# Kernel optimization log

Hardware: AMD Instinct MI355X
Metric: run time of the kernel (lower is better)

## Reference

```python
import jax, jax.numpy as jnp
import numpy as np

N, D, H, K, P = 1536, 1024, 16, 64, 8
FREQ_DIM = 14 * 3 * 128  # freq_embedding(pos, 128) flattened


def freq_embedding(t, size):
    # min_freq=0.01, max_freq=2**8 as in the block's call sites
    nf = size // 2
    freqs = (2.0 ** jnp.linspace(np.log2(0.01), np.log2(256.0), nf)).astype(jnp.float32)
    r = t[..., None] * freqs
    return jnp.stack((jnp.sin(r), jnp.cos(r)), axis=-1).reshape(t.shape[0], -1)


def layer_norm(x, eps=1e-5):
    m = jnp.mean(x, -1, keepdims=True)
    v = jnp.var(x, -1, keepdims=True)
    return (x - m) * jax.lax.rsqrt(v + eps)


def cond_norm(x, cond, ws, bs, wb, bb):
    return jax.nn.sigmoid(cond @ ws + bs) * layer_norm(x) + (cond @ wb + bb)


def _unit(v):
    return v * jax.lax.rsqrt(jnp.sum(v * v, -1, keepdims=True) + 1e-8)


def aa_frames(pos):
    # Gram-Schmidt frame from backbone N/CA/C (atom14 slots 0,1,2)
    n, ca, c = pos[:, 0], pos[:, 1], pos[:, 2]
    e1 = _unit(c - ca)
    v2 = n - ca
    e2 = _unit(v2 - jnp.sum(e1 * v2, -1, keepdims=True) * e1)
    e3 = jnp.cross(e1, e2)
    R = jnp.stack([e1, e2, e3], axis=-1)  # [N,3,3]
    return R, ca


def setup_inputs():
    key = jax.random.key(0)
    ks = iter(jax.random.split(key, 64))
    r = lambda *s: jax.random.normal(next(ks), s, jnp.float32)
    w = lambda *s: 0.02 * jax.random.normal(next(ks), s, jnp.float32)
    z = lambda *s: jnp.zeros(s, jnp.float32)
    return dict(
        local=r(N, D), pos=r(N, 14, 3), condition=r(N, D),
        mask=jnp.ones((N,), bool), pair_bias=r(H, N, N),
        w_f1=w(FREQ_DIM, 2 * D), b_f1=z(2 * D), w_f2=w(2 * D, D), b_f2=z(D),
        cn1_ws=w(D, D), cn1_bs=z(D), cn1_wb=w(D, D), cn1_bb=z(D),
        wq=w(D, H * K), wk=w(D, H * K), wv=w(D, H * K),
        wqp=w(D, H * P * 3), wkp=w(D, H * P * 3), wvp=w(D, H * P * 3),
        gamma=z(H), wo=w(H * (K + 4 * P), D), bo=z(D),
        cn2_ws=w(D, D), cn2_bs=z(D), cn2_wb=w(D, D), cn2_bb=z(D),
        wg1=w(D, 2 * D), bg1=z(2 * D), wg2=w(D, 2 * D), bg2=z(2 * D),
        wg3=w(2 * D, D), bg3=z(D),
        cn3_ws=w(D, D), cn3_bs=z(D), cn3_wb=w(D, D), cn3_bb=z(D),
        w_vel=w(D, 14 * 3),
    )


def reference(local, pos, condition, mask, pair_bias,
              w_f1, b_f1, w_f2, b_f2,
              cn1_ws, cn1_bs, cn1_wb, cn1_bb,
              wq, wk, wv, wqp, wkp, wvp, gamma, wo, bo,
              cn2_ws, cn2_bs, cn2_wb, cn2_bb,
              wg1, bg1, wg2, bg2, wg3, bg3,
              cn3_ws, cn3_bs, cn3_wb, cn3_bb, w_vel):
    n = local.shape[0]
    # embed_pred_pos: MLP over freq embedding of coords
    emb = freq_embedding(pos, 128)  # [N, 5376]
    local = local + (jax.nn.silu(emb @ w_f1 + b_f1) @ w_f2 + b_f2)
    # attention branch
    ai = cond_norm(local, condition, cn1_ws, cn1_bs, cn1_wb, cn1_bb)
    R, t = aa_frames(pos)
    q = (ai @ wq).reshape(n, H, K)
    k = (ai @ wk).reshape(n, H, K)
    v = (ai @ wv).reshape(n, H, K)
    to_glob = lambda p: jnp.einsum('nab,nhpb->nhpa', R, p) + t[:, None, None, :]
    qg = to_glob((ai @ wqp).reshape(n, H, P, 3))
    kg = to_glob((ai @ wkp).reshape(n, H, P, 3))
    vg = to_glob((ai @ wvp).reshape(n, H, P, 3))
    qk = jnp.einsum('ihk,jhk->hij', q, k) / np.sqrt(K).astype(np.float32)
    # squared point distances via norm expansion (never materialize [H,N,N,P,3])
    ptdot = jnp.einsum('ihpc,jhpc->hij', qg, kg)
    qn = jnp.sum(qg * qg, axis=(-1, -2)).T  # [H,N]
    kn = jnp.sum(kg * kg, axis=(-1, -2)).T
    dist2 = qn[:, :, None] + kn[None if False else slice(None), None, :] - 2.0 * ptdot
    wc = np.sqrt(2.0 / (9.0 * P)).astype(np.float32)
    logits = qk + pair_bias - 0.5 * wc * jax.nn.softplus(gamma)[:, None, None] * dist2
    logits = jnp.where(mask[None, None, :], logits, -1e9)
    a = jax.nn.softmax(logits, axis=-1)  # [H,N,N]
    o = jnp.einsum('hij,jhk->ihk', a, v).reshape(n, H * K)
    opg = jnp.einsum('hij,jhpc->ihpc', a, vg)
    opl = jnp.einsum('nba,nhpb->nhpa', R, opg - t[:, None, None, :])
    onorm = jnp.sqrt(jnp.sum(opl * opl, -1) + 1e-8).reshape(n, -1)
    upd = jnp.concatenate([o, opl.reshape(n, -1), onorm], axis=-1) @ wo + bo
    local = local + upd
    # gated MLP branch
    x = cond_norm(local, condition, cn2_ws, cn2_bs, cn2_wb, cn2_bb)
    local = local + (jax.nn.silu(x @ wg1 + bg1) * (x @ wg2 + bg2)) @ wg3 + bg3
    # output heads
    ln = cond_norm(local, condition, cn3_ws, cn3_bs, cn3_wb, cn3_bb)
    velocity = (ln @ w_vel).reshape(n, 14, 3)
    return local, velocity
```

## Files before the change

### kernel.cpp

```cpp
#include <hip/hip_runtime.h>
#include <hip/hip_bf16.h>
#include <math.h>

#define NRES 1536
#define NH 16
#define NNF 2359296ull
#define LOG2E 1.44269504f
#define KVS 4

typedef unsigned short u16;
typedef __attribute__((ext_vector_type(8))) short short8;
typedef __attribute__((ext_vector_type(4))) unsigned short u16x4;
typedef __attribute__((ext_vector_type(4))) float f32x4;

typedef const __attribute__((address_space(1))) void gvoid;
typedef __attribute__((address_space(3))) void lvoid;

__device__ __forceinline__ u16 f2b(float x){
    __hip_bfloat16 h = __float2bfloat16(x);
    return *reinterpret_cast<u16*>(&h);
}
__device__ __forceinline__ float b2f(u16 u){
    unsigned v = ((unsigned)u) << 16;
    return __uint_as_float(v);
}

#define F_BIAS  1
#define F_SILU  2
#define F_RESID 8
#define F_OUTBF 16

template<int TNF>
__global__ __launch_bounds__(256) void gemm_t(
    const u16* __restrict__ A, int lda, size_t zsA,
    const u16* __restrict__ BT, int ldb, size_t zsB,
    float* __restrict__ Cf, u16* __restrict__ Cb, int ldc, size_t zsC,
    const float* __restrict__ bias, size_t zsBias,
    const float* __restrict__ resid, int ldr, size_t zsR,
    int Ncols, int Kd, int flags, int ksl)
{
    constexpr int TN = TNF * 32;
    __shared__ u16 As[2][128 * 64];
    __shared__ u16 Bs[2][TN * 64];

    unsigned gx = gridDim.x, gy = gridDim.y;
    unsigned nb = gx * gy * gridDim.z;
    unsigned bid = (blockIdx.z * gy + blockIdx.y) * gx + blockIdx.x;
    if ((nb & 7u) == 0u) bid = (bid & 7u) * (nb >> 3) + (bid >> 3);
    const int bxi = bid % gx;
    const int byi = (bid / gx) % gy;
    const int bz  = bid / (gx * gy);

    const int tid = threadIdx.x;
    const int l = tid & 63, w = tid >> 6;
    const int bm = byi * 128, bn = bxi * TN;

    A  += zsA * bz;
    BT += zsB * bz;

    const int kbeg = ksl ? bz * ksl : 0;
    const int kend = ksl ? kbeg + ksl : Kd;
    const int nk = (kend - kbeg) >> 6;

    const int arow   = l >> 3;
    const int aslot  = l & 7;
    const int srcslt = aslot ^ arow;

    const u16* aBase[4];
    const u16* bBase[TN / 32];
    #pragma unroll
    for (int t = 0; t < 4; ++t) {
        int ra = bm + (w * 4 + t) * 8 + arow;
        aBase[t] = A + (size_t)ra * lda + srcslt * 8;
    }
    #pragma unroll
    for (int t = 0; t < TN / 32; ++t) {
        int rb = bn + (w * (TN / 32) + t) * 8 + arow;
        if (rb > Ncols - 1) rb = Ncols - 1;
        bBase[t] = BT + (size_t)rb * ldb + srcslt * 8;
    }

    const int wr = w >> 1, wc = w & 1;
    const int fr = l & 15;
    const int fq = l >> 4;

    f32x4 acc[4][TNF];
    #pragma unroll
    for (int i = 0; i < 4; ++i)
        #pragma unroll
        for (int j = 0; j < TNF; ++j) acc[i][j] = (f32x4){0.f, 0.f, 0.f, 0.f};

// ... 264 lines not shown

        float alpha[4];
        #pragma unroll
        for (int r = 0; r < 4; ++r) {
            float v = fmaxf(fmaxf(sacc[0][r], sacc[1][r]), fmaxf(sacc[2][r], sacc[3][r]));
            v = fmaxf(v, __shfl_xor(v, 1, 64));
            v = fmaxf(v, __shfl_xor(v, 2, 64));
            v = fmaxf(v, __shfl_xor(v, 4, 64));
            v = fmaxf(v, __shfl_xor(v, 8, 64));
            float mn = fmaxf(m_run[r], v);
            alpha[r] = exp2f((m_run[r] - mn) * LOG2E);
            m_run[r] = mn;
        }

        float psum[4] = {0.f, 0.f, 0.f, 0.f};
        #pragma unroll
        for (int n = 0; n < 4; ++n) {
            int col = n * 16 + fr;
            #pragma unroll
            for (int r = 0; r < 4; ++r) {
                float p = exp2f((sacc[n][r] - m_run[r]) * LOG2E);
                psum[r] += p;
                int rowf = w * 16 + fq * 4 + r;
                int byte = rowf * 128 + (((col >> 3) ^ (rowf & 7)) * 16) + (col & 7) * 2;
                *(u16*)((char*)Ps + byte) = f2b(p);
            }
        }
        #pragma unroll
        for (int r = 0; r < 4; ++r) {
            float v = psum[r];
            v += __shfl_xor(v, 1, 64);
            v += __shfl_xor(v, 2, 64);
            v += __shfl_xor(v, 4, 64);
            v += __shfl_xor(v, 8, 64);
            l_run[r] = l_run[r] * alpha[r] + v;
        }
        #pragma unroll
        for (int n = 0; n < 6; ++n)
            #pragma unroll
            for (int r = 0; r < 4; ++r)
                oacc[n][r] *= alpha[r];

        #pragma unroll
        for (int kk = 0; kk < 2; ++kk) {
            int prow = w * 16 + fr;
            short8 pa = *(const short8*)((const char*)Ps + prow * 128
                                         + (((kk * 4 + fq) ^ (prow & 7)) * 16));
            #pragma unroll
            for (int n = 0; n < 6; ++n) {
                int vrow = n * 16 + fr;
                short8 vv = *(const short8*)((const char*)Vs[cur] + vrow * 128
                                             + (((kk * 4 + fq) ^ (fr & 7)) * 16));
                oacc[n] = __builtin_amdgcn_mfma_f32_16x16x32_bf16(pa, vv, oacc[n], 0, 0, 0);
            }
        }

        __syncthreads();
        cur ^= 1;
        #pragma unroll
        for (int n = 0; n < 4; ++n) pbv[n] = pbn[n];
    }

    u16* Oz = Opart + ((size_t)z * NH + h) * NRES * 96;
    #pragma unroll
    for (int n = 0; n < 6; ++n) {
        int c = n * 16 + fr;
        #pragma unroll
        for (int r = 0; r < 4; ++r) {
            int row = q0 + w * 16 + fq * 4 + r;
            Oz[(size_t)row * 96 + c] = f2b(oacc[n][r]);
        }
    }
    if (fr == 0) {
        float* mlz = mlpart + ((size_t)z * NH + h) * NRES * 2;
        #pragma unroll
        for (int r = 0; r < 4; ++r) {
            int row = q0 + w * 16 + fq * 4 + r;
            mlz[row * 2 + 0] = m_run[r];
            mlz[row * 2 + 1] = l_run[r];
        }
    }
}

__global__ __launch_bounds__(256) void combine_kernel(
    const u16* __restrict__ Opart, const float* __restrict__ mlpart,
    float* __restrict__ cat)
{
    int idx = blockIdx.x * 256 + threadIdx.x;
    if (idx >= NH * NRES * 88) return;
    int c = idx % 88;
    int rh = idx / 88;
    float m[KVS], lv[KVS];
    float mm = -1e30f;
    #pragma unroll
    for (int s = 0; s < KVS; ++s) {
        size_t rr = (size_t)s * NH * NRES + rh;
        m[s] = mlpart[rr * 2];
        lv[s] = mlpart[rr * 2 + 1];
        mm = fmaxf(mm, m[s]);
    }
    float ll = 0.f, ov = 0.f;
    #pragma unroll
    for (int s = 0; s < KVS; ++s) {
        float wgt = exp2f((m[s] - mm) * LOG2E);
        ll += lv[s] * wgt;
        ov += b2f(Opart[((size_t)s * NH * NRES + rh) * 96 + c]) * wgt;
    }
    cat[(size_t)rh * 88 + c] = ov / ll;
}

struct TP9 { const float* p[9]; };

__global__ __launch_bounds__(256) void transpose_bz(
    TP9 tp, int ldi, size_t zsi,
    u16* __restrict__ out, int ldo, size_t zso, int K, int N, int nsrc)
{
    __shared__ float t[32][33];
    int z = blockIdx.z;
    const float* in = tp.p[(z < nsrc) ? z : 0] + zsi * ((z < nsrc) ? 0 : z);
    if (nsrc == 1) in = tp.p[0] + zsi * z;
    out += zso * z;
    int k0 = blockIdx.y * 32, n0 = blockIdx.x * 32;
    int tx = threadIdx.x & 31, ty = threadIdx.x >> 5;
    #pragma unroll
    for (int j = 0; j < 4; ++j) {
        int k = k0 + ty + j * 8;
        if (k < K && n0 + tx < N) t[ty + j * 8][tx] = in[(size_t)k * ldi + n0 + tx];
    }
    __syncthreads();
    #pragma unroll
    for (int j = 0; j < 4; ++j) {
        int n = n0 + ty + j * 8;
        int k = k0 + tx;
        if (n < N && k < K) out[(size_t)n * ldo + k] = f2b(t[tx][ty + j * 8]);
    }
}

__global__ __launch_bounds__(256) void f2b8_kernel(const float* __restrict__ in, u16* __restrict__ out, int n8)
{
    int i = blockIdx.x * 256 + threadIdx.x;
    if (i >= n8) return;
    size_t i0 = (size_t)i * 8;
    const float4* p = (const float4*)(in + i0);
    float4 a = p[0], b = p[1];
    short8 o;
    o[0]=(short)f2b(a.x); o[1]=(short)f2b(a.y); o[2]=(short)f2b(a.z); o[3]=(short)f2b(a.w);
    o[4]=(short)f2b(b.x); o[5]=(short)f2b(b.y); o[6]=(short)f2b(b.z); o[7]=(short)f2b(b.w);
    *(short8*)(out + i0) = o;
}

__global__ __launch_bounds__(256) void emb_kernel(const float* __restrict__ pos, u16* __restrict__ emb)
{
    int idx = blockIdx.x * 256 + threadIdx.x;
    int f = idx & 63;
    int rest = idx >> 6;
    int coord = rest % 42;
    int n = rest / 42;
    float t = pos[(size_t)n * 42 + coord];
    const double l0 = -6.643856189774724;
    const double step = 14.643856189774724 / 63.0;
    float freq = exp2f((float)(l0 + f * step));
    float r = t * freq;
    size_t o = (size_t)n * 5376 + (size_t)coord * 128 + 2 * f;
    emb[o]     = f2b(sinf(r));
    emb[o + 1] = f2b(cosf(r));
}

__global__ __launch_bounds__(256) void frames_kernel(const float* __restrict__ pos,
                                                     float* __restrict__ Rb, float* __restrict__ tb)
{
    int n = blockIdx.x * 256 + threadIdx.x;
    if (n >= NRES) return;
    const float* p = pos + (size_t)n * 42;
    float nx = p[0], ny = p[1], nz = p[2];
    float cax = p[3], cay = p[4], caz = p[5];
    float cx = p[6], cy = p[7], cz = p[8];
    float v1x = cx - cax, v1y = cy - cay, v1z = cz - caz;
    float i1 = rsqrtf(v1x * v1x + v1y * v1y + v1z * v1z + 1e-8f);
    float e1x = v1x * i1, e1y = v1y * i1, e1z = v1z * i1;
    float v2x = nx - cax, v2y = ny - cay, v2z = nz - caz;
    float d = e1x * v2x + e1y * v2y + e1z * v2z;
    float wx = v2x - d * e1x, wy = v2y - d * e1y, wz = v2z - d * e1z;
    float i2 = rsqrtf(wx * wx + wy * wy + wz * wz + 1e-8f);
    float e2x = wx * i2, e2y = wy * i2, e2z = wz * i2;
    float e3x = e1y * e2z - e1z * e2y;
    float e3y = e1z * e2x - e1x * e2z;
    float e3z = e1x * e2y - e1y * e2x;
    float* R = Rb + (size_t)n * 9;
    R[0] = e1x; R[1] = e2x; R[2] = e3x;
    R[3] = e1y; R[4] = e2y; R[5] = e3y;
    R[6] = e1z; R[7] = e2z; R[8] = e3z;
    tb[(size_t)n * 3 + 0] = cax;
    tb[(size_t)n * 3 + 1] = cay;
    tb[(size_t)n * 3 + 2] = caz;
}

__global__ __launch_bounds__(256) void bias_pack(const float* a, const float* b, const float* c,
                                                 const float* d, const float* e, const float* f,
                                                 float* out)
{
    int i = blockIdx.x * 256 + threadIdx.x;
    if (i >= 1024) return;
    out[i] = a[i]; out[1024 + i] = b[i]; out[2048 + i] = c[i];
    out[3072 + i] = d[i]; out[4096 + i] = e[i]; out[5120 + i] = f[i];
}

__global__ __launch_bounds__(256) void biasg_pack(const float* a, const float* b, float* out)
{
    int i = blockIdx.x * 256 + threadIdx.x;
    if (i >= 2048) return;
    out[i] = a[i]; out[2048 + i] = b[i];
}

__global__ __launch_bounds__(256) void glu_kernel(const u16* __restrict__ g12, u16* __restrict__ gm)
{
    int i = blockIdx.x * 256 + threadIdx.x;
    if (i >= NRES * 2048 / 8) return;
    size_t i0 = (size_t)i * 8;
    short8 a8 = *(const short8*)(g12 + i0);
    short8 b8 = *(const short8*)(g12 + (size_t)NRES * 2048 + i0);
    short8 o;
    #pragma unroll
    for (int j = 0; j < 8; ++j) {
        float a = b2f((u16)a8[j]);
        float b = b2f((u16)b8[j]);
        float s = a / (1.f + expf(-a));
        o[j] = (short)f2b(s * b);
    }
    *(short8*)(gm + i0) = o;
}

__global__ __launch_bounds__(256) void pack_qk(const float* __restrict__ qb, const float* __restrict__ kb,
                                               u16* __restrict__ qe, u16* __restrict__ ke)
{
    int idx = blockIdx.x * 256 + threadIdx.x;
    if (idx >= NH * NRES * 16) return;
    int g = idx & 15;
    int t = idx >> 4;
    int n = t % NRES;
    int h = t / NRES;
    size_t o = ((size_t)h * NRES + n) * 128 + g * 8;
    if (g < 8) {
        const float4* q4 = (const float4*)(qb + (size_t)n * 1024 + h * 64 + g * 8);
        const float4* k4 = (const float4*)(kb + (size_t)n * 1024 + h * 64 + g * 8);
        float4 qa = q4[0], qb2 = q4[1], ka = k4[0], kb2 = k4[1];
        short8 oq, ok;
        oq[0]=(short)f2b(0.125f*qa.x); oq[1]=(short)f2b(0.125f*qa.y);
        oq[2]=(short)f2b(0.125f*qa.z); oq[3]=(short)f2b(0.125f*qa.w);
        oq[4]=(short)f2b(0.125f*qb2.x); oq[5]=(short)f2b(0.125f*qb2.y);
        oq[6]=(short)f2b(0.125f*qb2.z); oq[7]=(short)f2b(0.125f*qb2.w);
        ok[0]=(short)f2b(ka.x); ok[1]=(short)f2b(ka.y); ok[2]=(short)f2b(ka.z); ok[3]=(short)f2b(ka.w);
        ok[4]=(short)f2b(kb2.x); ok[5]=(short)f2b(kb2.y); ok[6]=(short)f2b(kb2.z); ok[7]=(short)f2b(kb2.w);
        *(short8*)(qe + o) = oq;
        *(short8*)(ke + o) = ok;
    } else if (g >= 11) {
        short8 zz = {};
        *(short8*)(qe + o) = zz;
        *(short8*)(ke + o) = zz;
    }
}

__global__ __launch_bounds__(256) void build_pts(
    const float* __restrict__ qp, const float* __restrict__ kp, const float* __restrict__ vp,
    const float* __restrict__ Rb, const float* __restrict__ tb, const float* __restrict__ gamma,
    u16* __restrict__ qe, u16* __restrict__ ke, float* __restrict__ vgt)
{
    int idx = blockIdx.x * 256 + threadIdx.x;
    if (idx >= NRES * NH) return;
    int n = idx >> 4, h = idx & 15;
    float R[9];
    #pragma unroll
    for (int a = 0; a < 9; ++a) R[a] = Rb[(size_t)n * 9 + a];
    float t0 = tb[(size_t)n * 3 + 0], t1 = tb[(size_t)n * 3 + 1], t2 = tb[(size_t)n * 3 + 2];
    float g = gamma[h];
    float sp = (g > 20.f) ? g : log1pf(expf(g));
    float ch = 0.5f * (1.f / 6.f) * sp;

    u16* qeh = qe + ((size_t)h * NRES + n) * 128;
    u16* keh = ke + ((size_t)h * NRES + n) * 128;
    size_t pbase = (size_t)n * 384 + h * 24;
    float kn = 0.f;
    #pragma unroll
    for (int p = 0; p < 8; ++p) {
        size_t o = pbase + p * 3;
        {
            float x = qp[o], y = qp[o + 1], z = qp[o + 2];
            float g0 = R[0] * x + R[1] * y + R[2] * z + t0;
            float g1 = R[3] * x + R[4] * y + R[5] * z + t1;
            float g2 = R[6] * x + R[7] * y + R[8] * z + t2;
            qeh[64 + p * 3 + 0] = f2b(2.f * ch * g0);
            qeh[64 + p * 3 + 1] = f2b(2.f * ch * g1);
            qeh[64 + p * 3 + 2] = f2b(2.f * ch * g2);
        }
        {
            float x = kp[o], y = kp[o + 1], z = kp[o + 2];
            float g0 = R[0] * x + R[1] * y + R[2] * z + t0;
            float g1 = R[3] * x + R[4] * y + R[5] * z + t1;
            float g2 = R[6] * x + R[7] * y + R[8] * z + t2;
            keh[64 + p * 3 + 0] = f2b(g0);
            keh[64 + p * 3 + 1] = f2b(g1);
            keh[64 + p * 3 + 2] = f2b(g2);
            kn += g0 * g0 + g1 * g1 + g2 * g2;
        }
        {
            float x = vp[o], y = vp[o + 1], z = vp[o + 2];
            vgt[o]     = R[0] * x + R[1] * y + R[2] * z + t0;
            vgt[o + 1] = R[3] * x + R[4] * y + R[5] * z + t1;
            vgt[o + 2] = R[6] * x + R[7] * y + R[8] * z + t2;
        }
    }
    qeh[88] = f2b(1.0f);
    keh[88] = f2b(-ch * kn);
}

__global__ __launch_bounds__(256) void finalize_kernel(const float* __restrict__ cat,
                                                       const float* __restrict__ Rb,
                                                       const float* __restrict__ tb,
                                                       u16* __restrict__ featB)
{
    int idx = blockIdx.x * 256 + threadIdx.x;
    if (idx >= NRES * NH) return;
    int n = idx >> 4, h = idx & 15;
    float R[9];
    #pragma unroll
    for (int a = 0; a < 9; ++a) R[a] = Rb[(size_t)n * 9 + a];
    float t0 = tb[(size_t)n * 3 + 0], t1 = tb[(size_t)n * 3 + 1], t2 = tb[(size_t)n * 3 + 2];
    const float* c = cat + ((size_t)h * NRES + n) * 88;
    u16* fb = featB + (size_t)n * 1536;
    #pragma unroll
    for (int k = 0; k < 64; ++k) fb[h * 64 + k] = f2b(c[k]);
    #pragma unroll
    for (int p = 0; p < 8; ++p) {
        float x = c[64 + p * 3 + 0] - t0;
        float y = c[64 + p * 3 + 1] - t1;
        float z = c[64 + p * 3 + 2] - t2;
        float a0 = R[0] * x + R[3] * y + R[6] * z;
        float a1 = R[1] * x + R[4] * y + R[7] * z;
        float a2 = R[2] * x + R[5] * y + R[8] * z;
        fb[1024 + h * 24 + p * 3 + 0] = f2b(a0);
        fb[1024 + h * 24 + p * 3 + 1] = f2b(a1);
        fb[1024 + h * 24 + p * 3 + 2] = f2b(a2);
        fb[1408 + h * 8 + p] = f2b(sqrtf(a0 * a0 + a1 * a1 + a2 * a2 + 1e-8f));
    }
}

extern "C" void kernel_launch(void* const* d_in, const int* in_sizes, int n_in,
                              void* d_out, int out_size, void* d_ws, size_t ws_size,
                              hipStream_t stream)
{
    const float* local_in = (const float*)d_in[0];
    const float* pos      = (const float*)d_in[1];
    const float* cond     = (const float*)d_in[2];
    const float* pb       = (const float*)d_in[4];
    const float* w_f1     = (const float*)d_in[5];
    const float* b_f1     = (const float*)d_in[6];
    const float* w_f2     = (const float*)d_in[7];
    const float* b_f2     = (const float*)d_in[8];
    const float* cn1_ws   = (const float*)d_in[9];
    const float* cn1_bs   = (const float*)d_in[10];
    const float* cn1_wb   = (const float*)d_in[11];
    const float* cn1_bb   = (const float*)d_in[12];
    const float* wq       = (const float*)d_in[13];
    const float* wk       = (const float*)d_in[14];
    const float* wv       = (const float*)d_in[15];
    const float* wqp      = (const float*)d_in[16];
    const float* wkp      = (const float*)d_in[17];
    const float* wvp      = (const float*)d_in[18];
    const float* gamma    = (const float*)d_in[19];
    const float* wo       = (const float*)d_in[20];
    const float* bo       = (const float*)d_in[21];
    const float* cn2_ws   = (const float*)d_in[22];
    const float* cn2_bs   = (const float*)d_in[23];
    const float* cn2_wb   = (const float*)d_in[24];
    const float* cn2_bb   = (const float*)d_in[25];
    const float* wg1      = (const float*)d_in[26];
    const float* bg1      = (const float*)d_in[27];
    const float* wg2      = (const float*)d_in[28];
    const float* bg2      = (const float*)d_in[29];
    const float* wg3      = (const float*)d_in[30];
    const float* bg3      = (const float*)d_in[31];
    const float* cn3_ws   = (const float*)d_in[32];
    const float* cn3_bs   = (const float*)d_in[33];
    const float* cn3_wb   = (const float*)d_in[34];
    const float* cn3_bb   = (const float*)d_in[35];
    const float* w_vel    = (const float*)d_in[36];

    float* out = (float*)d_out;
    float* ws  = (float*)d_ws;

    size_t off = 0;
    auto alloc = [&](size_t nf) -> float* { float* p = ws + off; off += (nf + 7) & ~7ull; return p; };

    const size_t NN1 = (size_t)NRES * 1024;
    float* Rb    = alloc(NRES * 9);
    float* tb    = alloc(NRES * 3);
    float* loc   = alloc(NN1);
    u16*   cs6b  = (u16*)alloc(6 * NN1 / 2);
    u16*   condB = (u16*)alloc(NN1 / 2);
    u16*   normB = (u16*)alloc(NN1 / 2);
    float* bias2 = alloc(6 * 1024);
    float* biasg = alloc(2 * 2048);
    float* qb    = alloc(3 * NN1);
    float* kb    = qb + NN1;
    float* vb    = kb + NN1;
    float* qp    = alloc(3 * (size_t)NRES * 384);
    float* kp    = qp + NRES * 384;
    float* vp    = kp + NRES * 384;
    float* vgt   = alloc((size_t)NRES * 384);
    u16*   qeB   = (u16*)alloc((size_t)NH * NRES * 128 / 2);
    u16*   keB   = (u16*)alloc((size_t)NH * NRES * 128 / 2);
    u16*   vTB   = (u16*)alloc((size_t)NH * 96 * NRES / 2);
    float* cat   = alloc((size_t)NH * NRES * 88);
    u16*   featB = (u16*)alloc((size_t)NRES * 1536 / 2);
    u16*   g1sB  = (u16*)alloc((size_t)NRES * 2048 / 2);
    u16*   gmB   = (u16*)alloc((size_t)NRES * 2048 / 2);
    u16*   cnT9  = (u16*)alloc((size_t)9 * 1024 * 1024 / 2);
    u16*   ptsT  = (u16*)alloc((size_t)3 * 384 * 1024 / 2);
    u16*   wgT   = (u16*)alloc((size_t)2 * 2048 * 1024 / 2);
    u16*   wf1T  = (u16*)alloc((size_t)2048 * 5376 / 2);
    u16*   wf2T  = (u16*)alloc((size_t)1024 * 2048 / 2);
    u16*   woT   = (u16*)alloc((size_t)1024 * 1536 / 2);
    u16*   wg3T  = (u16*)alloc((size_t)1024 * 2048 / 2);
    u16*   wvT   = (u16*)alloc((size_t)42 * 1024 / 2 + 8);
    u16*   embB  = (u16*)alloc((size_t)NRES * 5376 / 2);
    u16*   hidB  = (u16*)alloc((size_t)NRES * 2048 / 2);
    u16*   pscr  = (u16*)alloc((size_t)2 * NRES * 2048 * 4 / 2);
    u16*   Opart = (u16*)alloc((size_t)KVS * NH * NRES * 96 / 2);
    float* mlprt = alloc((size_t)KVS * NH * NRES * 2);

    const float* nilf = nullptr;

    auto gemm = [&](int tnf, const u16* A, int lda, size_t zsA,
                    const u16* BT, int ldb, size_t zsB,
                    float* Cf, u16* Cb2, int ldc, size_t zsC,
                    const float* bias, size_t zsBias,
                    const float* resid, int ldr, size_t zsR,
                    int Nc, int Kd, int flags, int gz, int ksl) {
        int tn = tnf * 32;
        dim3 grid((Nc + tn - 1) / tn, NRES / 128, gz);
        if (tnf == 4)
            hipLaunchKernelGGL(gemm_t<4>, grid, dim3(256), 0, stream,
                               A, lda, zsA, BT, ldb, zsB, Cf, Cb2, ldc, zsC,
                               bias, zsBias, resid, ldr, zsR, Nc, Kd, flags, ksl);
        else
            hipLaunchKernelGGL(gemm_t<2>, grid, dim3(256), 0, stream,
                               A, lda, zsA, BT, ldb, zsB, Cf, Cb2, ldc, zsC,
                               bias, zsBias, resid, ldr, zsR, Nc, Kd, flags, ksl);
    };
    auto red = [&](const u16* part, size_t slice, int nsl, float* Cf, u16* Cb2,
                   const float* bias, const float* resid, int ldr, int Nc, int flags) {
        hipLaunchKernelGGL(reduce_epi, dim3(1024), dim3(256), 0, stream,
                           part, slice, nsl, Cf, Cb2, bias, resid, ldr, NRES, Nc, flags);
    };
    auto redcn = [&](const u16* part, size_t slice, int nsl,
                     const float* bias, const float* resid, float* locOut, int cnIdx) {
        hipLaunchKernelGGL(reduce_cn, dim3(NRES), dim3(256), 0, stream,
                           part, slice, nsl, bias, resid, locOut,
                           cs6b + (size_t)(2 * cnIdx) * NN1,
                           cs6b + (size_t)(2 * cnIdx + 1) * NN1, normB);
    };
    auto tpz = [&](TP9 tp, int ldi, int K, int N, u16* o, int ldo, size_t zso, int nsrc) {
        dim3 grid((N + 31) / 32, (K + 31) / 32, nsrc);
        hipLaunchKernelGGL(transpose_bz, grid, dim3(256), 0, stream, tp, ldi, (size_t)0, o, ldo, zso, K, N, nsrc);
    };
    auto tps = [&](const float* in, int ldi, size_t zsi, int K, int N, u16* o, int ldo, size_t zso, int gz) {
        dim3 grid((N + 31) / 32, (K + 31) / 32, gz);
        TP9 tp; tp.p[0] = in;
        hipLaunchKernelGGL(transpose_bz, grid, dim3(256), 0, stream, tp, ldi, zsi, o, ldo, zso, K, N, 1);
    };

    hipLaunchKernelGGL(frames_kernel, dim3(6), dim3(256), 0, stream, pos, Rb, tb);
    hipLaunchKernelGGL(emb_kernel, dim3((NRES * 42 * 64) / 256), dim3(256), 0, stream, pos, embB);
    hipLaunchKernelGGL(f2b8_kernel, dim3(768), dim3(256), 0, stream, cond, condB, NRES * 1024 / 8);
    hipLaunchKernelGGL(bias_pack, dim3(4), dim3(256), 0, stream,
                       cn1_bs, cn1_bb, cn2_bs, cn2_bb, cn3_bs, cn3_bb, bias2);
    hipLaunchKernelGGL(biasg_pack, dim3(8), dim3(256), 0, stream, bg1, bg2, biasg);

    {
        TP9 t9; t9.p[0]=cn1_ws; t9.p[1]=cn1_wb; t9.p[2]=cn2_ws; t9.p[3]=cn2_wb;
        t9.p[4]=cn3_ws; t9.p[5]=cn3_wb; t9.p[6]=wq; t9.p[7]=wk; t9.p[8]=wv;
        tpz(t9, 1024, 1024, 1024, cnT9, 1024, (size_t)1024 * 1024, 9);
    }
    {
        TP9 t3; t3.p[0]=wqp; t3.p[1]=wkp; t3.p[2]=wvp;
        tpz(t3, 384, 1024, 384, ptsT, 1024, (size_t)384 * 1024, 3);
    }
    {
        TP9 t2; t2.p[0]=wg1; t2.p[1]=wg2;
        tpz(t2, 2048, 1024, 2048, wgT, 1024, (size_t)2048 * 1024, 2);
    }
    tps(w_f1, 2048, 0, 5376, 2048, wf1T, 5376, 0, 1);
    tps(w_f2, 1024, 0, 2048, 1024, wf2T, 2048, 0, 1);
    tps(wo,   1024, 0, 1536, 1024, woT,  1536, 0, 1);
    tps(wg3,  1024, 0, 2048, 1024, wg3T, 2048, 0, 1);
    tps(w_vel,  42, 0, 1024,   42, wvT,  1024, 0, 1);

    gemm(2, condB, 1024, 0, cnT9, 1024, (size_t)1024 * 1024, nullptr, cs6b, 1024, NN1,
         bias2, 1024, nilf, 0, 0, 1024, 1024, F_BIAS | F_OUTBF, 6, 0);

    gemm(2, embB, 5376, 0, wf1T, 5376, 0, nullptr, pscr, 2048, (size_t)NRES * 2048,
         nilf, 0, nilf, 0, 0, 2048, 5376, F_OUTBF, 4, 1344);
    red(pscr, (size_t)NRES * 2048, 4, nullptr, hidB, b_f1, nilf, 0,
        2048, F_BIAS | F_SILU | F_OUTBF);
    gemm(2, hidB, 2048, 0, wf2T, 2048, 0, nullptr, pscr, 1024, NN1,
         nilf, 0, nilf, 0, 0, 1024, 2048, F_OUTBF, 4, 512);
    redcn(pscr, NN1, 4, b_f2, local_in, loc, 0);

    gemm(2, normB, 1024, 0, cnT9 + (size_t)6 * 1024 * 1024, 1024, (size_t)1024 * 1024,
         qb, nullptr, 1024, NN1, nilf, 0, nilf, 0, 0, 1024, 1024, 0, 3, 0);
    gemm(2, normB, 1024, 0, ptsT, 1024, (size_t)384 * 1024, qp, nullptr, 384, (size_t)NRES * 384,
         nilf, 0, nilf, 0, 0, 384, 1024, 0, 3, 0);

    hipMemsetAsync(vTB, 0, (size_t)NH * 96 * NRES * 2, stream);
    hipLaunchKernelGGL(pack_qk, dim3((NH * NRES * 16 + 255) / 256), dim3(256), 0, stream, qb, kb, qeB, keB);
    hipLaunchKernelGGL(build_pts, dim3(96), dim3(256), 0, stream,
                       qp, kp, vp, Rb, tb, gamma, qeB, keB, vgt);
    tps(vb, 1024, 64, NRES, 64, vTB, NRES, (size_t)96 * NRES, NH);
    tps(vgt, 384, 24, NRES, 24, vTB + (size_t)64 * NRES, NRES, (size_t)96 * NRES, NH);

    hipLaunchKernelGGL(attn_kernel, dim3(NRES / 64, NH, KVS), dim3(256), 0, stream,
                       qeB, keB, vTB, pb, Opart, mlprt);
    hipLaunchKernelGGL(combine_kernel, dim3((NH * NRES * 88 + 255) / 256), dim3(256), 0, stream,
                       Opart, mlprt, cat);
    hipLaunchKernelGGL(finalize_kernel, dim3(96), dim3(256), 0, stream, cat, Rb, tb, featB);

    gemm(2, featB, 1536, 0, woT, 1536, 0, nullptr, pscr, 1024, NN1,
         nilf, 0, nilf, 0, 0, 1024, 1536, F_OUTBF, 4, 384);
    redcn(pscr, NN1, 4, bo, loc, loc, 1);

    gemm(2, normB, 1024, 0, wgT, 1024, (size_t)2048 * 1024, nullptr, g1sB, 2048, (size_t)NRES * 2048,
         biasg, 2048, nilf, 0, 0, 2048, 1024, F_BIAS | F_OUTBF, 2, 0);
    u16* gmO = embB;
    hipLaunchKernelGGL(glu_kernel, dim3((NRES * 2048 / 8 + 255) / 256), dim3(256), 0, stream, g1sB, gmO);
    gemm(2, gmO, 2048, 0, wg3T, 2048, 0, nullptr, pscr, 1024, NN1,
         nilf, 0, nilf, 0, 0, 1024, 2048, F_OUTBF, 4, 512);
    redcn(pscr, NN1, 4, bg3, loc, out, 2);

    gemm(2, normB, 1024, 0, wvT, 1024, 0, nullptr, pscr, 42, (size_t)NRES * 42,
         nilf, 0, nilf, 0, 0, 42, 1024, F_OUTBF, 8, 128);
    red(pscr, (size_t)NRES * 42, 8, out + (size_t)NRES * 1024, nullptr,
        nilf, nilf, 0, 42, 0);
}
```

Before: 507.7 us.

## Fuse prologue kernels, merge QKV and point projections, fuse combine with finalize

Five small setup kernels (frames, embedding, condition cast, two bias packs) become one block-partitioned prologue launch. The Q/K/V and point projections become a single wide GEMM into a 4224-column buffer. That relies on the point-weight transpose sitting contiguously after the wq/wk/wv transposes. Q/K packing and point building are merged into one launch, and the two V transposes plus the memset are replaced by one vt_pack kernel. The split-KV combine now also does the frame rotation and writes bf16 features directly, removing the fp32 intermediate. The cost is far less parallelism in that combine step: 96 blocks with one thread per (row, head) doing strided, uncoalesced reads.

```diff
diff --git a/kernel.cpp b/kernel.cpp
--- a/kernel.cpp
+++ b/kernel.cpp
@@ -7,6 +7,7 @@
 #define NNF 2359296ull
 #define LOG2E 1.44269504f
 #define KVS 4
+#define LDQ 4224
 
 typedef unsigned short u16;
 typedef __attribute__((ext_vector_type(8))) short short8;
@@ -437,31 +438,69 @@
     }
 }
 
-__global__ __launch_bounds__(256) void combine_kernel(
+__global__ __launch_bounds__(256) void combine_fin(
     const u16* __restrict__ Opart, const float* __restrict__ mlpart,
-    float* __restrict__ cat)
+    const float* __restrict__ Rb, const float* __restrict__ tb,
+    u16* __restrict__ featB)
 {
     int idx = blockIdx.x * 256 + threadIdx.x;
-    if (idx >= NH * NRES * 88) return;
-    int c = idx % 88;
-    int rh = idx / 88;
-    float m[KVS], lv[KVS];
+    if (idx >= NRES * NH) return;
+    int n = idx >> 4, h = idx & 15;
+
+    float m[KVS], lv[KVS], wgt[KVS];
     float mm = -1e30f;
     #pragma unroll
     for (int s = 0; s < KVS; ++s) {
-        size_t rr = (size_t)s * NH * NRES + rh;
+        size_t rr = ((size_t)s * NH + h) * NRES + n;
         m[s] = mlpart[rr * 2];
         lv[s] = mlpart[rr * 2 + 1];
         mm = fmaxf(mm, m[s]);
     }
-    float ll = 0.f, ov = 0.f;
+    float ll = 0.f;
     #pragma unroll
     for (int s = 0; s < KVS; ++s) {
-        float wgt = exp2f((m[s] - mm) * LOG2E);
-        ll += lv[s] * wgt;
-        ov += b2f(Opart[((size_t)s * NH * NRES + rh) * 96 + c]) * wgt;
-    }
-    cat[(size_t)rh * 88 + c] = ov / ll;
+        wgt[s] = exp2f((m[s] - mm) * LOG2E);
+        ll += lv[s] * wgt[s];
+    }
+    float inv = 1.f / ll;
+    const u16* op[KVS];
+    #pragma unroll
+    for (int s = 0; s < KVS; ++s)
+        op[s] = Opart + (((size_t)s * NH + h) * NRES + n) * 96;
+
+    u16* fb = featB + (size_t)n * 1536;
+    #pragma unroll
+    for (int k = 0; k < 64; ++k) {
+        float v = 0.f;
+        #pragma unroll
+        for (int s = 0; s < KVS; ++s) v += b2f(op[s][k]) * wgt[s];
+        fb[h * 64 + k] = f2b(v * inv);
+    }
+
+    float R[9];
+    #pragma unroll
+    for (int a = 0; a < 9; ++a) R[a] = Rb[(size_t)n * 9 + a];
+    float t0 = tb[(size_t)n * 3 + 0], t1 = tb[(size_t)n * 3 + 1], t2 = tb[(size_t)n * 3 + 2];
+    #pragma unroll
+    for (int p = 0; p < 8; ++p) {
+        float d[3];
+        #pragma unroll
+        for (int dd = 0; dd < 3; ++dd) {
+            int c = 64 + p * 3 + dd;
+            float v = 0.f;
+            #pragma unroll
+            for (int s = 0; s < KVS; ++s) v += b2f(op[s][c]) * wgt[s];
+            d[dd] = v * inv;
+        }
+        float x = d[0] - t0, y = d[1] - t1, z = d[2] - t2;
+        float a0 = R[0] * x + R[3] * y + R[6] * z;
+        float a1 = R[1] * x + R[4] * y + R[7] * z;
+        float a2 = R[2] * x + R[5] * y + R[8] * z;
+        fb[1024 + h * 24 + p * 3 + 0] = f2b(a0);
+        fb[1024 + h * 24 + p * 3 + 1] = f2b(a1);
+        fb[1024 + h * 24 + p * 3 + 2] = f2b(a2);
+        fb[1408 + h * 8 + p] = f2b(sqrtf(a0 * a0 + a1 * a1 + a2 * a2 + 1e-8f));
+    }
 }
 
 struct TP9 { const float* p[9]; };
@@ -491,136 +530,136 @@
     }
 }
 
-__global__ __launch_bounds__(256) void f2b8_kernel(const float* __restrict__ in, u16* __restrict__ out, int n8)
-{
-    int i = blockIdx.x * 256 + threadIdx.x;
-    if (i >= n8) return;
-    size_t i0 = (size_t)i * 8;
-    const float4* p = (const float4*)(in + i0);
-    float4 a = p[0], b = p[1];
-    short8 o;
-    o[0]=(short)f2b(a.x); o[1]=(short)f2b(a.y); o[2]=(short)f2b(a.z); o[3]=(short)f2b(a.w);
-    o[4]=(short)f2b(b.x); o[5]=(short)f2b(b.y); o[6]=(short)f2b(b.z); o[7]=(short)f2b(b.w);
-    *(short8*)(out + i0) = o;
-}
-
-__global__ __launch_bounds__(256) void emb_kernel(const float* __restrict__ pos, u16* __restrict__ emb)
-{
-    int idx = blockIdx.x * 256 + threadIdx.x;
-    int f = idx & 63;
-    int rest = idx >> 6;
-    int coord = rest % 42;
-    int n = rest / 42;
-    float t = pos[(size_t)n * 42 + coord];
-    const double l0 = -6.643856189774724;
-    const double step = 14.643856189774724 / 63.0;
-    float freq = exp2f((float)(l0 + f * step));
-    float r = t * freq;
-    size_t o = (size_t)n * 5376 + (size_t)coord * 128 + 2 * f;
-    emb[o]     = f2b(sinf(r));
-    emb[o + 1] = f2b(cosf(r));
-}
-
-__global__ __launch_bounds__(256) void frames_kernel(const float* __restrict__ pos,
-                                                     float* __restrict__ Rb, float* __restrict__ tb)
-{
-    int n = blockIdx.x * 256 + threadIdx.x;
-    if (n >= NRES) return;
-    const float* p = pos + (size_t)n * 42;
-    float nx = p[0], ny = p[1], nz = p[2];
-    float cax = p[3], cay = p[4], caz = p[5];
-    float cx = p[6], cy = p[7], cz = p[8];
-    float v1x = cx - cax, v1y = cy - cay, v1z = cz - caz;
-    float i1 = rsqrtf(v1x * v1x + v1y * v1y + v1z * v1z + 1e-8f);
-    float e1x = v1x * i1, e1y = v1y * i1, e1z = v1z * i1;
-    float v2x = nx - cax, v2y = ny - cay, v2z = nz - caz;
-    float d = e1x * v2x + e1y * v2y + e1z * v2z;
-    float wx = v2x - d * e1x, wy = v2y - d * e1y, wz = v2z - d * e1z;
-    float i2 = rsqrtf(wx * wx + wy * wy + wz * wz + 1e-8f);
-    float e2x = wx * i2, e2y = wy * i2, e2z = wz * i2;
-    float e3x = e1y * e2z - e1z * e2y;
-    float e3y = e1z * e2x - e1x * e2z;
-    float e3z = e1x * e2y - e1y * e2x;
-    float* R = Rb + (size_t)n * 9;
-    R[0] = e1x; R[1] = e2x; R[2] = e3x;
-    R[3] = e1y; R[4] = e2y; R[5] = e3y;
-    R[6] = e1z; R[7] = e2z; R[8] = e3z;
-    tb[(size_t)n * 3 + 0] = cax;
-    tb[(size_t)n * 3 + 1] = cay;
-    tb[(size_t)n * 3 + 2] = caz;
-}
-
-__global__ __launch_bounds__(256) void bias_pack(const float* a, const float* b, const float* c,
-                                                 const float* d, const float* e, const float* f,
-                                                 float* out)
-{
-    int i = blockIdx.x * 256 + threadIdx.x;
-    if (i >= 1024) return;
-    out[i] = a[i]; out[1024 + i] = b[i]; out[2048 + i] = c[i];
-    out[3072 + i] = d[i]; out[4096 + i] = e[i]; out[5120 + i] = f[i];
-}
-
-__global__ __launch_bounds__(256) void biasg_pack(const float* a, const float* b, float* out)
-{
-    int i = blockIdx.x * 256 + threadIdx.x;
-    if (i >= 2048) return;
-    out[i] = a[i]; out[2048 + i] = b[i];
-}
-
-__global__ __launch_bounds__(256) void glu_kernel(const u16* __restrict__ g12, u16* __restrict__ gm)
-{
-    int i = blockIdx.x * 256 + threadIdx.x;
-    if (i >= NRES * 2048 / 8) return;
-    size_t i0 = (size_t)i * 8;
-    short8 a8 = *(const short8*)(g12 + i0);
-    short8 b8 = *(const short8*)(g12 + (size_t)NRES * 2048 + i0);
-    short8 o;
-    #pragma unroll
-    for (int j = 0; j < 8; ++j) {
-        float a = b2f((u16)a8[j]);
-        float b = b2f((u16)b8[j]);
-        float s = a / (1.f + expf(-a));
-        o[j] = (short)f2b(s * b);
-    }
-    *(short8*)(gm + i0) = o;
-}
-
-__global__ __launch_bounds__(256) void pack_qk(const float* __restrict__ qb, const float* __restrict__ kb,
-                                               u16* __restrict__ qe, u16* __restrict__ ke)
-{
-    int idx = blockIdx.x * 256 + threadIdx.x;
-    if (idx >= NH * NRES * 16) return;
-    int g = idx & 15;
-    int t = idx >> 4;
-    int n = t % NRES;
-    int h = t / NRES;
-    size_t o = ((size_t)h * NRES + n) * 128 + g * 8;
-    if (g < 8) {
-        const float4* q4 = (const float4*)(qb + (size_t)n * 1024 + h * 64 + g * 8);
-        const float4* k4 = (const float4*)(kb + (size_t)n * 1024 + h * 64 + g * 8);
-        float4 qa = q4[0], qb2 = q4[1], ka = k4[0], kb2 = k4[1];
-        short8 oq, ok;
-        oq[0]=(short)f2b(0.125f*qa.x); oq[1]=(short)f2b(0.125f*qa.y);
-        oq[2]=(short)f2b(0.125f*qa.z); oq[3]=(short)f2b(0.125f*qa.w);
-        oq[4]=(short)f2b(0.125f*qb2.x); oq[5]=(short)f2b(0.125f*qb2.y);
-        oq[6]=(short)f2b(0.125f*qb2.z); oq[7]=(short)f2b(0.125f*qb2.w);
-        ok[0]=(short)f2b(ka.x); ok[1]=(short)f2b(ka.y); ok[2]=(short)f2b(ka.z); ok[3]=(short)f2b(ka.w);
-        ok[4]=(short)f2b(kb2.x); ok[5]=(short)f2b(kb2.y); ok[6]=(short)f2b(kb2.z); ok[7]=(short)f2b(kb2.w);
-        *(short8*)(qe + o) = oq;
-        *(short8*)(ke + o) = ok;
-    } else if (g >= 11) {
-        short8 zz = {};
-        *(short8*)(qe + o) = zz;
-        *(short8*)(ke + o) = zz;
-    }
-}
-
-__global__ __launch_bounds__(256) void build_pts(
-    const float* __restrict__ qp, const float* __restrict__ kp, const float* __restrict__ vp,
-    const float* __restrict__ Rb, const float* __restrict__ tb, const float* __restrict__ gamma,
+__global__ __launch_bounds__(256) void vt_pack(
+    const float* __restrict__ qkc, const float* __restrict__ vgt,
+    u16* __restrict__ vt)
+{
+    __shared__ float t[32][33];
+    int h = blockIdx.z, grp = blockIdx.y, n0 = blockIdx.x * 32;
+    int tx = threadIdx.x & 31, ty = threadIdx.x >> 5;
+    #pragma unroll
+    for (int j = 0; j < 4; ++j) {
+        int n = n0 + ty + j * 8;
+        int c = grp * 32 + tx;
+        float v = 0.f;
+        if (c < 64) v = qkc[(size_t)n * LDQ + 2048 + h * 64 + c];
+        else if (c < 88) v = vgt[(size_t)n * 384 + h * 24 + (c - 64)];
+        t[ty + j * 8][tx] = v;
+    }
+    __syncthreads();
+    #pragma unroll
+    for (int j = 0; j < 4; ++j) {
+        int r = grp * 32 + ty + j * 8;
+        vt[((size_t)h * 96 + r) * NRES + n0 + tx] = f2b(t[tx][ty + j * 8]);
+    }
+}
+
+__global__ __launch_bounds__(256) void prologue_kernel(
+    const float* __restrict__ pos, const float* __restrict__ cond,
+    const float* __restrict__ cn1_bs, const float* __restrict__ cn1_bb,
+    const float* __restrict__ cn2_bs, const float* __restrict__ cn2_bb,
+    const float* __restrict__ cn3_bs, const float* __restrict__ cn3_bb,
+    const float* __restrict__ bg1, const float* __restrict__ bg2,
+    float* __restrict__ Rb, float* __restrict__ tb,
+    u16* __restrict__ emb, u16* __restrict__ condB,
+    float* __restrict__ bias2, float* __restrict__ biasg)
+{
+    int b = blockIdx.x, tid = threadIdx.x;
+    if (b < 16128) {
+        int idx = b * 256 + tid;
+        int f = idx & 63;
+        int rest = idx >> 6;
+        int coord = rest % 42;
+        int n = rest / 42;
+        float t = pos[(size_t)n * 42 + coord];
+        const double l0 = -6.643856189774724;
+        const double step = 14.643856189774724 / 63.0;
+        float freq = exp2f((float)(l0 + f * step));
+        float r = t * freq;
+        size_t o = (size_t)n * 5376 + (size_t)coord * 128 + 2 * f;
+        emb[o]     = f2b(sinf(r));
+        emb[o + 1] = f2b(cosf(r));
+    } else if (b < 16896) {
+        int i = (b - 16128) * 256 + tid;
+        size_t i0 = (size_t)i * 8;
+        const float4* p = (const float4*)(cond + i0);
+        float4 a = p[0], bb = p[1];
+        short8 o;
+        o[0]=(short)f2b(a.x); o[1]=(short)f2b(a.y); o[2]=(short)f2b(a.z); o[3]=(short)f2b(a.w);
+        o[4]=(short)f2b(bb.x); o[5]=(short)f2b(bb.y); o[6]=(short)f2b(bb.z); o[7]=(short)f2b(bb.w);
+        *(short8*)(condB + i0) = o;
+    } else if (b < 16902) {
+        int n = (b - 16896) * 256 + tid;
+        if (n >= NRES) return;
+        const float* p = pos + (size_t)n * 42;
+        float nx = p[0], ny = p[1], nz = p[2];
+        float cax = p[3], cay = p[4], caz = p[5];
+        float cx = p[6], cy = p[7], cz = p[8];
+        float v1x = cx - cax, v1y = cy - cay, v1z = cz - caz;
+        float i1 = rsqrtf(v1x * v1x + v1y * v1y + v1z * v1z + 1e-8f);
+        float e1x = v1x * i1, e1y = v1y * i1, e1z = v1z * i1;
+        float v2x = nx - cax, v2y = ny - cay, v2z = nz - caz;
+        float d = e1x * v2x + e1y * v2y + e1z * v2z;
+        float wx = v2x - d * e1x, wy = v2y - d * e1y, wz = v2z - d * e1z;
+        float i2 = rsqrtf(wx * wx + wy * wy + wz * wz + 1e-8f);
+        float e2x = wx * i2, e2y = wy * i2, e2z = wz * i2;
+        float e3x = e1y * e2z - e1z * e2y;
+        float e3y = e1z * e2x - e1x * e2z;
+        float e3z = e1x * e2y - e1y * e2x;
+        float* R = Rb + (size_t)n * 9;
+        R[0] = e1x; R[1] = e2x; R[2] = e3x;
+        R[3] = e1y; R[4] = e2y; R[5] = e3y;
+        R[6] = e1z; R[7] = e2z; R[8] = e3z;
+        tb[(size_t)n * 3 + 0] = cax;
+        tb[(size_t)n * 3 + 1] = cay;
+        tb[(size_t)n * 3 + 2] = caz;
+    } else if (b < 16906) {
+        int i = (b - 16902) * 256 + tid;
+        if (i >= 1024) return;
+        bias2[i] = cn1_bs[i]; bias2[1024 + i] = cn1_bb[i]; bias2[2048 + i] = cn2_bs[i];
+        bias2[3072 + i] = cn2_bb[i]; bias2[4096 + i] = cn3_bs[i]; bias2[5120 + i] = cn3_bb[i];
+    } else {
+        int i = (b - 16906) * 256 + tid;
+        if (i >= 2048) return;
+        biasg[i] = bg1[i]; biasg[2048 + i] = bg2[i];
+    }
+}
+
+__global__ __launch_bounds__(256) void pack_attn(
+    const float* __restrict__ qkc,
+    const float* __restrict__ Rb, const float* __restrict__ tb,
+    const float* __restrict__ gamma,
     u16* __restrict__ qe, u16* __restrict__ ke, float* __restrict__ vgt)
 {
-    int idx = blockIdx.x * 256 + threadIdx.x;
+    int b = blockIdx.x;
+    if (b < 1536) {
+        int idx = b * 256 + threadIdx.x;
+        int g = idx & 15;
+        int t = idx >> 4;
+        int n = t % NRES;
+        int h = t / NRES;
+        size_t o = ((size_t)h * NRES + n) * 128 + g * 8;
+        if (g < 8) {
+            const float4* q4 = (const float4*)(qkc + (size_t)n * LDQ + h * 64 + g * 8);
+            const float4* k4 = (const float4*)(qkc + (size_t)n * LDQ + 1024 + h * 64 + g * 8);
+            float4 qa = q4[0], qb2 = q4[1], ka = k4[0], kb2 = k4[1];
+            short8 oq, ok;
+            oq[0]=(short)f2b(0.125f*qa.x); oq[1]=(short)f2b(0.125f*qa.y);
+            oq[2]=(short)f2b(0.125f*qa.z); oq[3]=(short)f2b(0.125f*qa.w);
+            oq[4]=(short)f2b(0.125f*qb2.x); oq[5]=(short)f2b(0.125f*qb2.y);
+            oq[6]=(short)f2b(0.125f*qb2.z); oq[7]=(short)f2b(0.125f*qb2.w);
+            ok[0]=(short)f2b(ka.x); ok[1]=(short)f2b(ka.y); ok[2]=(short)f2b(ka.z); ok[3]=(short)f2b(ka.w);
+            ok[4]=(short)f2b(kb2.x); ok[5]=(short)f2b(kb2.y); ok[6]=(short)f2b(kb2.z); ok[7]=(short)f2b(kb2.w);
+            *(short8*)(qe + o) = oq;
+            *(short8*)(ke + o) = ok;
+        } else if (g >= 11) {
+            short8 zz = {};
+            *(short8*)(qe + o) = zz;
+            *(short8*)(ke + o) = zz;
+        }
+        return;
+    }
+    int idx = (b - 1536) * 256 + threadIdx.x;
     if (idx >= NRES * NH) return;
     int n = idx >> 4, h = idx & 15;
     float R[9];
@@ -633,13 +672,14 @@
 
     u16* qeh = qe + ((size_t)h * NRES + n) * 128;
     u16* keh = ke + ((size_t)h * NRES + n) * 128;
-    size_t pbase = (size_t)n * 384 + h * 24;
+    const float* qp = qkc + (size_t)n * LDQ + 3072 + h * 24;
+    const float* kp = qkc + (size_t)n * LDQ + 3456 + h * 24;
+    const float* vp = qkc + (size_t)n * LDQ + 3840 + h * 24;
     float kn = 0.f;
     #pragma unroll
     for (int p = 0; p < 8; ++p) {
-        size_t o = pbase + p * 3;
         {
-            float x = qp[o], y = qp[o + 1], z = qp[o + 2];
+            float x = qp[p*3], y = qp[p*3+1], z = qp[p*3+2];
             float g0 = R[0] * x + R[1] * y + R[2] * z + t0;
             float g1 = R[3] * x + R[4] * y + R[5] * z + t1;
             float g2 = R[6] * x + R[7] * y + R[8] * z + t2;
@@ -648,7 +688,7 @@
             qeh[64 + p * 3 + 2] = f2b(2.f * ch * g2);
         }
         {
-            float x = kp[o], y = kp[o + 1], z = kp[o + 2];
+            float x = kp[p*3], y = kp[p*3+1], z = kp[p*3+2];
             float g0 = R[0] * x + R[1] * y + R[2] * z + t0;
             float g1 = R[3] * x + R[4] * y + R[5] * z + t1;
             float g2 = R[6] * x + R[7] * y + R[8] * z + t2;
@@ -658,45 +698,32 @@
             kn += g0 * g0 + g1 * g1 + g2 * g2;
         }
         {
-            float x = vp[o], y = vp[o + 1], z = vp[o + 2];
-            vgt[o]     = R[0] * x + R[1] * y + R[2] * z + t0;
-            vgt[o + 1] = R[3] * x + R[4] * y + R[5] * z + t1;
-            vgt[o + 2] = R[6] * x + R[7] * y + R[8] * z + t2;
+            float x = vp[p*3], y = vp[p*3+1], z = vp[p*3+2];
+            vgt[(size_t)n * 384 + h * 24 + p * 3 + 0] = R[0] * x + R[1] * y + R[2] * z + t0;
+            vgt[(size_t)n * 384 + h * 24 + p * 3 + 1] = R[3] * x + R[4] * y + R[5] * z + t1;
+            vgt[(size_t)n * 384 + h * 24 + p * 3 + 2] = R[6] * x + R[7] * y + R[8] * z + t2;
         }
     }
     qeh[88] = f2b(1.0f);
     keh[88] = f2b(-ch * kn);
 }
 
-__global__ __launch_bounds__(256) void finalize_kernel(const float* __restrict__ cat,
-                                                       const float* __restrict__ Rb,
-                                                       const float* __restrict__ tb,
-                                                       u16* __restrict__ featB)
-{
-    int idx = blockIdx.x * 256 + threadIdx.x;
-    if (idx >= NRES * NH) return;
-    int n = idx >> 4, h = idx & 15;
-    float R[9];
-    #pragma unroll
-    for (int a = 0; a < 9; ++a) R[a] = Rb[(size_t)n * 9 + a];
-    float t0 = tb[(size_t)n * 3 + 0], t1 = tb[(size_t)n * 3 + 1], t2 = tb[(size_t)n * 3 + 2];
-    const float* c = cat + ((size_t)h * NRES + n) * 88;
-    u16* fb = featB + (size_t)n * 1536;
-    #pragma unroll
-    for (int k = 0; k < 64; ++k) fb[h * 64 + k] = f2b(c[k]);
-    #pragma unroll
-    for (int p = 0; p < 8; ++p) {
-        float x = c[64 + p * 3 + 0] - t0;
-        float y = c[64 + p * 3 + 1] - t1;
-        float z = c[64 + p * 3 + 2] - t2;
-        float a0 = R[0] * x + R[3] * y + R[6] * z;
-        float a1 = R[1] * x + R[4] * y + R[7] * z;
-        float a2 = R[2] * x + R[5] * y + R[8] * z;
-        fb[1024 + h * 24 + p * 3 + 0] = f2b(a0);
-        fb[1024 + h * 24 + p * 3 + 1] = f2b(a1);
-        fb[1024 + h * 24 + p * 3 + 2] = f2b(a2);
-        fb[1408 + h * 8 + p] = f2b(sqrtf(a0 * a0 + a1 * a1 + a2 * a2 + 1e-8f));
-    }
+__global__ __launch_bounds__(256) void glu_kernel(const u16* __restrict__ g12, u16* __restrict__ gm)
+{
+    int i = blockIdx.x * 256 + threadIdx.x;
+    if (i >= NRES * 2048 / 8) return;
+    size_t i0 = (size_t)i * 8;
+    short8 a8 = *(const short8*)(g12 + i0);
+    short8 b8 = *(const short8*)(g12 + (size_t)NRES * 2048 + i0);
+    short8 o;
+    #pragma unroll
+    for (int j = 0; j < 8; ++j) {
+        float a = b2f((u16)a8[j]);
+        float b = b2f((u16)b8[j]);
+        float s = a / (1.f + expf(-a));
+        o[j] = (short)f2b(s * b);
+    }
+    *(short8*)(gm + i0) = o;
 }
 
 extern "C" void kernel_launch(void* const* d_in, const int* in_sizes, int n_in,
@@ -755,17 +782,11 @@
     u16*   normB = (u16*)alloc(NN1 / 2);
     float* bias2 = alloc(6 * 1024);
     float* biasg = alloc(2 * 2048);
-    float* qb    = alloc(3 * NN1);
-    float* kb    = qb + NN1;
-    float* vb    = kb + NN1;
-    float* qp    = alloc(3 * (size_t)NRES * 384);
-    float* kp    = qp + NRES * 384;
-    float* vp    = kp + NRES * 384;
+    float* qkc   = alloc((size_t)NRES * LDQ);
     float* vgt   = alloc((size_t)NRES * 384);
     u16*   qeB   = (u16*)alloc((size_t)NH * NRES * 128 / 2);
     u16*   keB   = (u16*)alloc((size_t)NH * NRES * 128 / 2);
     u16*   vTB   = (u16*)alloc((size_t)NH * 96 * NRES / 2);
-    float* cat   = alloc((size_t)NH * NRES * 88);
     u16*   featB = (u16*)alloc((size_t)NRES * 1536 / 2);
     u16*   g1sB  = (u16*)alloc((size_t)NRES * 2048 / 2);
     u16*   gmB   = (u16*)alloc((size_t)NRES * 2048 / 2);
@@ -824,12 +845,9 @@
         hipLaunchKernelGGL(transpose_bz, grid, dim3(256), 0, stream, tp, ldi, zsi, o, ldo, zso, K, N, 1);
     };
 
-    hipLaunchKernelGGL(frames_kernel, dim3(6), dim3(256), 0, stream, pos, Rb, tb);
-    hipLaunchKernelGGL(emb_kernel, dim3((NRES * 42 * 64) / 256), dim3(256), 0, stream, pos, embB);
-    hipLaunchKernelGGL(f2b8_kernel, dim3(768), dim3(256), 0, stream, cond, condB, NRES * 1024 / 8);
-    hipLaunchKernelGGL(bias_pack, dim3(4), dim3(256), 0, stream,
-                       cn1_bs, cn1_bb, cn2_bs, cn2_bb, cn3_bs, cn3_bb, bias2);
-    hipLaunchKernelGGL(biasg_pack, dim3(8), dim3(256), 0, stream, bg1, bg2, biasg);
+    hipLaunchKernelGGL(prologue_kernel, dim3(16914), dim3(256), 0, stream,
+                       pos, cond, cn1_bs, cn1_bb, cn2_bs, cn2_bb, cn3_bs, cn3_bb,
+                       bg1, bg2, Rb, tb, embB, condB, bias2, biasg);
 
     {
         TP9 t9; t9.p[0]=cn1_ws; t9.p[1]=cn1_wb; t9.p[2]=cn2_ws; t9.p[3]=cn2_wb;
@@ -861,23 +879,18 @@
          nilf, 0, nilf, 0, 0, 1024, 2048, F_OUTBF, 4, 512);
     redcn(pscr, NN1, 4, b_f2, local_in, loc, 0);
 
-    gemm(2, normB, 1024, 0, cnT9 + (size_t)6 * 1024 * 1024, 1024, (size_t)1024 * 1024,
-         qb, nullptr, 1024, NN1, nilf, 0, nilf, 0, 0, 1024, 1024, 0, 3, 0);
-    gemm(2, normB, 1024, 0, ptsT, 1024, (size_t)384 * 1024, qp, nullptr, 384, (size_t)NRES * 384,
-         nilf, 0, nilf, 0, 0, 384, 1024, 0, 3, 0);
-
-    hipMemsetAsync(vTB, 0, (size_t)NH * 96 * NRES * 2, stream);
-    hipLaunchKernelGGL(pack_qk, dim3((NH * NRES * 16 + 255) / 256), dim3(256), 0, stream, qb, kb, qeB, keB);
-    hipLaunchKernelGGL(build_pts, dim3(96), dim3(256), 0, stream,
-                       qp, kp, vp, Rb, tb, gamma, qeB, keB, vgt);
-    tps(vb, 1024, 64, NRES, 64, vTB, NRES, (size_t)96 * NRES, NH);
-    tps(vgt, 384, 24, NRES, 24, vTB + (size_t)64 * NRES, NRES, (size_t)96 * NRES, NH);
+    gemm(2, normB, 1024, 0, cnT9 + (size_t)6 * 1024 * 1024, 1024, 0,
+         qkc, nullptr, LDQ, 0, nilf, 0, nilf, 0, 0, LDQ, 1024, 0, 1, 0);
+
+    hipLaunchKernelGGL(pack_attn, dim3(1536 + 96), dim3(256), 0, stream,
+                       qkc, Rb, tb, gamma, qeB, keB, vgt);
+    hipLaunchKernelGGL(vt_pack, dim3(NRES / 32, 3, NH), dim3(256), 0, stream,
+                       qkc, vgt, vTB);
 
     hipLaunchKernelGGL(attn_kernel, dim3(NRES / 64, NH, KVS), dim3(256), 0, stream,
                        qeB, keB, vTB, pb, Opart, mlprt);
-    hipLaunchKernelGGL(combine_kernel, dim3((NH * NRES * 88 + 255) / 256), dim3(256), 0, stream,
-                       Opart, mlprt, cat);
-    hipLaunchKernelGGL(finalize_kernel, dim3(96), dim3(256), 0, stream, cat, Rb, tb, featB);
+    hipLaunchKernelGGL(combine_fin, dim3(96), dim3(256), 0, stream,
+                       Opart, mlprt, Rb, tb, featB);
 
     gemm(2, featB, 1536, 0, woT, 1536, 0, nullptr, pscr, 1024, NN1,
          nilf, 0, nilf, 0, 0, 1024, 1536, F_OUTBF, 4, 384);
```

After: 487.3 us. -4.0%, faster.
